# Performance work log

Measured on AMD Instinct MI355X. Metric: run time of the kernel, lower is better.

## Reference

```python
import jax, jax.numpy as jnp
import numpy as np

WH, WW = 7, 7
N = WH * WW
NH = 6
HEAD_DIM = 192 // NH
W_RES = 56
R_MAX = 4 * 56  # patch_size[0] * H
PI = 3.141592653589793


def _rel_coords():
    ch, cw = np.arange(WH), np.arange(WW)
    coords = np.stack(np.meshgrid(ch, cw, indexing='ij'))  # (2, WH, WW)
    flat = coords.reshape(2, -1)
    rel = flat[:, :, None] - flat[:, None, :]  # (2, N, N)
    radius = rel[0]   # in [-(WH-1), WH-1]
    azimuth = rel[1]  # in [-(WW-1), WW-1]
    return radius, azimuth


def setup_inputs() -> dict:
    key = jax.random.key(0)
    ks = jax.random.split(key, 10)
    B_ = 2048
    dim = 192
    return {
        'x': jax.random.normal(ks[0], (B_, N, dim), jnp.float32),
        'D': jax.random.uniform(ks[1], (B_, 1), jnp.float32),
        'qkv_w': jax.random.normal(ks[2], (3 * dim, dim), jnp.float32) * 0.02,
        'qkv_b': jax.random.normal(ks[3], (3 * dim,), jnp.float32) * 0.02,
        'proj_w': jax.random.normal(ks[4], (dim, dim), jnp.float32) * 0.02,
        'proj_b': jax.random.normal(ks[5], (dim,), jnp.float32) * 0.02,
        'a_p': jax.random.normal(ks[6], (2 * WW - 1, NH), jnp.float32) * 0.02,
        'b_p': jax.random.normal(ks[7], (2 * WW - 1, NH), jnp.float32) * 0.02,
        'a_r': jax.random.normal(ks[8], (2 * WH - 1, NH), jnp.float32) * 0.02,
        'b_r': jax.random.normal(ks[9], (2 * WH - 1, NH), jnp.float32) * 0.02,
    }


def reference(x, D, qkv_w, qkv_b, proj_w, proj_b, a_p, b_p, a_r, b_r):
    B_, n, C = x.shape
    radius_np, azimuth_np = _rel_coords()
    # torch a_r[radius] with negative ints wraps like python indexing; emulate via modulo
    rad_idx = jnp.asarray(radius_np % (2 * WH - 1))
    az_idx = jnp.asarray(azimuth_np % (2 * WW - 1))
    radius = jnp.asarray(radius_np, jnp.float32)   # (N, N)
    azimuth = jnp.asarray(azimuth_np, jnp.float32)  # (N, N)

    scale = HEAD_DIM ** -0.5
    qkv = (x @ qkv_w.T + qkv_b).reshape(B_, n, 3, NH, HEAD_DIM)
    qkv = jnp.transpose(qkv, (2, 0, 3, 1, 4))  # (3, B_, NH, N, hd)
    q, k, v = qkv[0] * scale, qkv[1], qkv[2]

    attn = jnp.einsum('bhnd,bhmd->bhnm', q, k)  # (B_, NH, N, N)

    # azimuthal bias: (N, N, NH) -> (NH, N, N)
    az = azimuth * (2.0 * PI / W_RES)
    A_phi = a_p[az_idx] * jnp.cos(az)[..., None] + b_p[az_idx] * jnp.sin(az)[..., None]
    A_phi = jnp.transpose(A_phi, (2, 0, 1))  # (NH, N, N)

    # radial bias: D (B_,1) scales radius -> (B_, N, N); combine -> (B_, NH, N, N)
    rad = D[:, 0][:, None, None] * radius[None]  # (B_, N, N)
    ang = rad * (2.0 * PI / R_MAX)
    A_r = (a_r[rad_idx][None] * jnp.cos(ang)[..., None]
           + b_r[rad_idx][None] * jnp.sin(ang)[..., None])  # (B_, N, N, NH)
    A_r = jnp.transpose(A_r, (0, 3, 1, 2))  # (B_, NH, N, N)

    attn = jax.nn.softmax(attn + A_phi[None] + A_r, axis=-1)
    out = jnp.einsum('bhnm,bhmd->bhnd', attn, v)
    out = jnp.transpose(out, (0, 2, 1, 3)).reshape(B_, n, C)
    return out @ proj_w.T + proj_b
```

## Files before the change

### kernel.cpp

```cpp
#include <hip/hip_runtime.h>

#define NTOK 49
#define NH 6
#define HD 32
#define DIM 192
#define QKV_DIM 576
#define PI_F 3.14159265358979323846f

typedef __bf16 bf16_t;
typedef __bf16 bf16x4 __attribute__((ext_vector_type(4)));
typedef __bf16 bf16x8 __attribute__((ext_vector_type(8)));
typedef float f32x4 __attribute__((ext_vector_type(4)));

__global__ __launch_bounds__(256) void cvt_weights(const float* __restrict__ qkv_w,
                                                   const float* __restrict__ proj_w,
                                                   bf16_t* __restrict__ wq,
                                                   bf16_t* __restrict__ wp) {
    int idx = blockIdx.x * 256 + threadIdx.x;
    if (idx < QKV_DIM * DIM) {
        wq[idx] = (bf16_t)qkv_w[idx];
    } else {
        int j = idx - QKV_DIM * DIM;
        if (j < DIM * DIM) wp[j] = (bf16_t)proj_w[j];
    }
}

__device__ __forceinline__ int2 pack4(float a, float b, float c, float d) {
    bf16x4 t = { (bf16_t)a, (bf16_t)b, (bf16_t)c, (bf16_t)d };
    union { bf16x4 v; int2 i; } u;
    u.v = t;
    return u.i;
}

__device__ __forceinline__ bf16x8 asm_frag(int2 p0, int2 p1, int src_lo, bool sel_hi) {
    int a0x = __shfl(p0.x, src_lo),      a0y = __shfl(p0.y, src_lo);
    int a1x = __shfl(p0.x, src_lo + 16), a1y = __shfl(p0.y, src_lo + 16);
    int b0x = __shfl(p1.x, src_lo),      b0y = __shfl(p1.y, src_lo);
    int b1x = __shfl(p1.x, src_lo + 16), b1y = __shfl(p1.y, src_lo + 16);
    union { int x[4]; bf16x8 v; } u;
    u.x[0] = sel_hi ? b0x : a0x;
    u.x[1] = sel_hi ? b0y : a0y;
    u.x[2] = sel_hi ? b1x : a1x;
    u.x[3] = sel_hi ? b1y : a1y;
    return u.v;
}

__global__ __launch_bounds__(384, 3) void fused_win_attn(
        const float* __restrict__ x,
        const float* __restrict__ Dp,
        const bf16_t* __restrict__ wq,
        const float* __restrict__ qkv_b,
        const bf16_t* __restrict__ wp,
        const float* __restrict__ proj_b,
        const float* __restrict__ a_p,
        const float* __restrict__ b_p,
        const float* __restrict__ a_r,
        const float* __restrict__ b_r,
        float* __restrict__ out) {
    __shared__ __align__(16) bf16_t sh_xo[49 * 200];
    __shared__ __align__(16) bf16_t vt_sh[NH][32 * 72];
    __shared__ float bias_sh[NH][169];

    const int tid  = threadIdx.x;
    const int w    = tid >> 6;
    const int lane = tid & 63;
    const int l16  = lane & 15;
    const int quad = lane >> 4;
    const int win  = blockIdx.x;

    bf16_t* vt     = vt_sh[w];
    float*  bias13 = bias_sh[w];

    const float* xg = x + (size_t)win * (NTOK * DIM);
    for (int u = tid; u < 2352; u += 384) {
        int e = u * 4;
        int r = e / 192, c = e % 192;
        float4 xv = *(const float4*)(xg + e);
        bf16x4 pk = { (bf16_t)xv.x, (bf16_t)xv.y, (bf16_t)xv.z, (bf16_t)xv.w };
        *(bf16x4*)(&sh_xo[r * 200 + c]) = pk;
    }

    const float Dv = Dp[win];
    for (int u = lane; u < 169; u += 64) {
        int dr = u / 13 - 6, da = u % 13 - 6;
        int ri = (dr < 0) ? dr + 13 : dr;
        int ai = (da < 0) ? da + 13 : da;
        float ang_a = (float)da * (2.0f * PI_F / 56.0f);
        float ang_r = Dv * (float)dr * (2.0f * PI_F / 448.0f);
        bias13[u] = a_p[ai * NH + w] * __cosf(ang_a) + b_p[ai * NH + w] * __sinf(ang_a)
                  + a_r[ri * NH + w] * __cosf(ang_r) + b_r[ri * NH + w] * __sinf(ang_r);
    }
    __syncthreads();

    int xoff[4];
#pragma unroll
    for (int mt = 0; mt < 4; ++mt) {
        int row = mt * 16 + l16;
        xoff[mt] = min(row, 48) * 200 + quad * 8;
    }

    const float scale = 0.17677669529663687f;
    int2 qp[4][2], kp[4][2];
    {
        const bf16_t* wgq = wq + (size_t)(w * 32) * DIM;
        const bf16_t* wgk = wq + (size_t)(DIM + w * 32) * DIM;
        f32x4 qa[4][2] = {}, ka[4][2] = {};
#pragma unroll
        for (int ks = 0; ks < 6; ++ks) {
            bf16x8 wq0 = *(const bf16x8*)(wgq + (size_t)l16 * DIM + ks * 32 + quad * 8);
            bf16x8 wq1 = *(const bf16x8*)(wgq + (size_t)(16 + l16) * DIM + ks * 32 + quad * 8);
            bf16x8 wk0 = *(const bf16x8*)(wgk + (size_t)l16 * DIM + ks * 32 + quad * 8);
            bf16x8 wk1 = *(const bf16x8*)(wgk + (size_t)(16 + l16) * DIM + ks * 32 + quad * 8);
#pragma unroll
            for (int mt = 0; mt < 4; ++mt) {
                bf16x8 xf = *(const bf16x8*)(&sh_xo[xoff[mt] + ks * 32]);
                qa[mt][0] = __builtin_amdgcn_mfma_f32_16x16x32_bf16(wq0, xf, qa[mt][0], 0, 0, 0);
                qa[mt][1] = __builtin_amdgcn_mfma_f32_16x16x32_bf16(wq1, xf, qa[mt][1], 0, 0, 0);
                ka[mt][0] = __builtin_amdgcn_mfma_f32_16x16x32_bf16(wk0, xf, ka[mt][0], 0, 0, 0);
                ka[mt][1] = __builtin_amdgcn_mfma_f32_16x16x32_bf16(wk1, xf, ka[mt][1], 0, 0, 0);
            }
        }
        float4 bq0 = *(const float4*)(qkv_b + w * 32 + quad * 4);
        float4 bq1 = *(const float4*)(qkv_b + w * 32 + 16 + quad * 4);
        float4 bk0 = *(const float4*)(qkv_b + DIM + w * 32 + quad * 4);
        float4 bk1 = *(const float4*)(qkv_b + DIM + w * 32 + 16 + quad * 4);
#pragma unroll
        for (int mt = 0; mt < 4; ++mt) {
            qp[mt][0] = pack4((qa[mt][0][0] + bq0.x) * scale, (qa[mt][0][1] + bq0.y) * scale,
                              (qa[mt][0][2] + bq0.z) * scale, (qa[mt][0][3] + bq0.w) * scale);
            qp[mt][1] = pack4((qa[mt][1][0] + bq1.x) * scale, (qa[mt][1][1] + bq1.y) * scale,
                              (qa[mt][1][2] + bq1.z) * scale, (qa[mt][1][3] + bq1.w) * scale);
            kp[mt][0] = pack4(ka[mt][0][0] + bk0.x, ka[mt][0][1] + bk0.y,
                              ka[mt][0][2] + bk0.z, ka[mt][0][3] + bk0.w);
            kp[mt][1] = pack4(ka[mt][1][0] + bk1.x, ka[mt][1][1] + bk1.y,
                              ka[mt][1][2] + bk1.z, ka[mt][1][3] + bk1.w);
        }
    }
    {
        const bf16_t* wgv = wq + (size_t)(2 * DIM + w * 32) * DIM;
        f32x4 va[4][2] = {};
#pragma unroll
        for (int ks = 0; ks < 6; ++ks) {
            bf16x8 wv0 = *(const bf16x8*)(wgv + (size_t)l16 * DIM + ks * 32 + quad * 8);
            bf16x8 wv1 = *(const bf16x8*)(wgv + (size_t)(16 + l16) * DIM + ks * 32 + quad * 8);
#pragma unroll
            for (int mt = 0; mt < 4; ++mt) {
                bf16x8 xf = *(const bf16x8*)(&sh_xo[xoff[mt] + ks * 32]);
                va[mt][0] = __builtin_amdgcn_mfma_f32_16x16x32_bf16(xf, wv0, va[mt][0], 0, 0, 0);
                va[mt][1] = __builtin_amdgcn_mfma_f32_16x16x32_bf16(xf, wv1, va[mt][1], 0, 0, 0);
            }
        }
        float bv0 = qkv_b[2 * DIM + w * 32 + l16];
        float bv1 = qkv_b[2 * DIM + w * 32 + 16 + l16];
#pragma unroll
        for (int mt = 0; mt < 4; ++mt) {
            *(int2*)(&vt[l16 * 72 + mt * 16 + quad * 4]) =
                pack4(va[mt][0][0] + bv0, va[mt][0][1] + bv0, va[mt][0][2] + bv0, va[mt][0][3] + bv0);
            *(int2*)(&vt[(16 + l16) * 72 + mt * 16 + quad * 4]) =
                pack4(va[mt][1][0] + bv1, va[mt][1][1] + bv1, va[mt][1][2] + bv1, va[mt][1][3] + bv1);
        }
    }

    const int src_lo  = ((lane >> 4) & 1) * 32 + l16;
    const bool sel_hi = (lane & 32) != 0;
    bf16x8 qf[4], kf[4];
#pragma unroll
    for (int t = 0; t < 4; ++t) {
        qf[t] = asm_frag(qp[t][0], qp[t][1], src_lo, sel_hi);
        kf[t] = asm_frag(kp[t][0], kp[t][1], src_lo, sel_hi);
    }
    bf16x8 vf[2][2];
#pragma unroll
    for (int ntd = 0; ntd < 2; ++ntd)
#pragma unroll
        for (int kt = 0; kt < 2; ++kt)
            vf[ntd][kt] = *(const bf16x8*)(&vt[(ntd * 16 + l16) * 72 + kt * 32 + quad * 8]);

    int jcp[4];
#pragma unroll
    for (int nt = 0; nt < 4; ++nt) {
        int p = 0;
#pragma unroll
        for (int r = 0; r < 4; ++r) {
            int j = nt * 16 + quad * 4 + r;
            p |= ((j / 7) * 13 + (j % 7)) << (8 * r);
        }
        jcp[nt] = p;
    }

    __syncthreads();

    for (int mt = 0; mt < 4; ++mt) {
        f32x4 s[4] = {};
#pragma unroll
        for (int nt = 0; nt < 4; ++nt)
            s[nt] = __builtin_amdgcn_mfma_f32_16x16x32_bf16(kf[nt], qf[mt], s[nt], 0, 0, 0);

        int i = mt * 16 + l16;
        int icl = min(i, 48);
        int icode = (icl / 7) * 13 + (icl % 7) + 84;

        float val[4][4];
        float mx = -1e30f;
#pragma unroll
        for (int nt = 0; nt < 4; ++nt)
#pragma unroll
            for (int r = 0; r < 4; ++r) {
                int j = nt * 16 + quad * 4 + r;
                int idx = icode - ((jcp[nt] >> (8 * r)) & 255);
                idx = max(idx, 0);
                float vv = s[nt][r] + bias13[idx];
                vv = (j < 49) ? vv : -1e30f;
                val[nt][r] = vv;
                mx = fmaxf(mx, vv);
            }
        mx = fmaxf(mx, __shfl_xor(mx, 16));
        mx = fmaxf(mx, __shfl_xor(mx, 32));
        float sum = 0.f;
#pragma unroll
        for (int nt = 0; nt < 4; ++nt)
#pragma unroll
            for (int r = 0; r < 4; ++r) {
                float e = __expf(val[nt][r] - mx);
                val[nt][r] = e;
                sum += e;
            }
        sum += __shfl_xor(sum, 16);
        sum += __shfl_xor(sum, 32);
        float rs = 1.0f / sum;

        int2 pv0 = pack4(val[0][0], val[0][1], val[0][2], val[0][3]);
        int2 pv1 = pack4(val[1][0], val[1][1], val[1][2], val[1][3]);
        int2 pv2 = pack4(val[2][0], val[2][1], val[2][2], val[2][3]);
        int2 pv3 = pack4(val[3][0], val[3][1], val[3][2], val[3][3]);
        bf16x8 pT0 = asm_frag(pv0, pv1, src_lo, sel_hi);
        bf16x8 pT1 = asm_frag(pv2, pv3, src_lo, sel_hi);

        f32x4 o0 = {}, o1 = {};
        o0 = __builtin_amdgcn_mfma_f32_16x16x32_bf16(vf[0][0], pT0, o0, 0, 0, 0);
        o0 = __builtin_amdgcn_mfma_f32_16x16x32_bf16(vf[0][1], pT1, o0, 0, 0, 0);
        o1 = __builtin_amdgcn_mfma_f32_16x16x32_bf16(vf[1][0], pT0, o1, 0, 0, 0);
        o1 = __builtin_amdgcn_mfma_f32_16x16x32_bf16(vf[1][1], pT1, o1, 0, 0, 0);

        if (i < 49) {
            *(int2*)(&sh_xo[i * 200 + w * 32 + quad * 4]) =
                pack4(o0[0] * rs, o0[1] * rs, o0[2] * rs, o0[3] * rs);
            *(int2*)(&sh_xo[i * 200 + w * 32 + 16 + quad * 4]) =
                pack4(o1[0] * rs, o1[1] * rs, o1[2] * rs, o1[3] * rs);
        }
    }

    __syncthreads();

    bf16x8 wf[2][6];
#pragma unroll
    for (int nt = 0; nt < 2; ++nt)
#pragma unroll
        for (int ks = 0; ks < 6; ++ks)
            wf[nt][ks] = *(const bf16x8*)(wp + (size_t)(w * 32 + nt * 16 + l16) * DIM + ks * 32 + quad * 8);

    f32x4 pacc[4][2] = {};
#pragma unroll
    for (int mt = 0; mt < 4; ++mt)
#pragma unroll
        for (int ks = 0; ks < 6; ++ks) {
            bf16x8 oa = *(const bf16x8*)(&sh_xo[xoff[mt] + ks * 32]);
            pacc[mt][0] = __builtin_amdgcn_mfma_f32_16x16x32_bf16(oa, wf[0][ks], pacc[mt][0], 0, 0, 0);
            pacc[mt][1] = __builtin_amdgcn_mfma_f32_16x16x32_bf16(oa, wf[1][ks], pacc[mt][1], 0, 0, 0);
        }

    float pb0 = proj_b[w * 32 + l16];
    float pb1 = proj_b[w * 32 + 16 + l16];
#pragma unroll
    for (int mt = 0; mt < 4; ++mt)
#pragma unroll
        for (int r = 0; r < 4; ++r) {
            int i = mt * 16 + quad * 4 + r;
            if (i < 49) {
                float* op = out + ((size_t)win * NTOK + i) * DIM + w * 32;
                op[l16]      = pacc[mt][0][r] + pb0;
                op[16 + l16] = pacc[mt][1][r] + pb1;
            }
        }
}

extern "C" void kernel_launch(void* const* d_in, const int* in_sizes, int n_in,
                              void* d_out, int out_size, void* d_ws, size_t ws_size,
                              hipStream_t stream) {
    const float* x      = (const float*)d_in[0];
    const float* D      = (const float*)d_in[1];
    const float* qkv_w  = (const float*)d_in[2];
    const float* qkv_b  = (const float*)d_in[3];
    const float* proj_w = (const float*)d_in[4];
    const float* proj_b = (const float*)d_in[5];
    const float* a_p    = (const float*)d_in[6];
    const float* b_p    = (const float*)d_in[7];
    const float* a_r    = (const float*)d_in[8];
    const float* b_r    = (const float*)d_in[9];
    float* out = (float*)d_out;

    const int B_ = in_sizes[0] / (NTOK * DIM);

    char* wsp = (char*)d_ws;
    bf16_t* wq = (bf16_t*)wsp; wsp += (size_t)QKV_DIM * DIM * 2;
    bf16_t* wp = (bf16_t*)wsp;

    cvt_weights<<<dim3((QKV_DIM * DIM + DIM * DIM + 255) / 256), dim3(256), 0, stream>>>(
        qkv_w, proj_w, wq, wp);

    fused_win_attn<<<dim3(B_), dim3(384), 0, stream>>>(
        x, D, wq, qkv_b, wp, proj_b, a_p, b_p, a_r, b_r, out);
}
```

Before: 302.6 us.

## Process two windows per 768-thread block and keep V fragments in registers

```diff
diff --git a/kernel.cpp b/kernel.cpp
--- a/kernel.cpp
+++ b/kernel.cpp
@@ -6,6 +6,7 @@
 #define DIM 192
 #define QKV_DIM 576
 #define PI_F 3.14159265358979323846f
+#define XSTR 204
 
 typedef __bf16 bf16_t;
 typedef __bf16 bf16x4 __attribute__((ext_vector_type(4)));
@@ -45,7 +46,7 @@
     return u.v;
 }
 
-__global__ __launch_bounds__(384, 3) void fused_win_attn(
+__global__ __launch_bounds__(768, 3) void fused_win_attn(
         const float* __restrict__ x,
         const float* __restrict__ Dp,
         const bf16_t* __restrict__ wq,
@@ -56,39 +57,44 @@
         const float* __restrict__ b_p,
         const float* __restrict__ a_r,
         const float* __restrict__ b_r,
-        float* __restrict__ out) {
-    __shared__ __align__(16) bf16_t sh_xo[49 * 200];
-    __shared__ __align__(16) bf16_t vt_sh[NH][32 * 72];
-    __shared__ float bias_sh[NH][169];
+        float* __restrict__ out,
+        int nwin) {
+    __shared__ __align__(16) bf16_t sh_xo[2][49 * XSTR];
+    __shared__ float bias_sh[12][169];
 
     const int tid  = threadIdx.x;
     const int w    = tid >> 6;
     const int lane = tid & 63;
     const int l16  = lane & 15;
     const int quad = lane >> 4;
-    const int win  = blockIdx.x;
-
-    bf16_t* vt     = vt_sh[w];
+    const int wb   = w / 6;
+    const int h    = w % 6;
+    const int win  = blockIdx.x * 2 + wb;
+    const int winc = min(win, nwin - 1);
+    const bool alive = (win < nwin);
+
+    bf16_t* xl     = sh_xo[wb];
     float*  bias13 = bias_sh[w];
 
-    const float* xg = x + (size_t)win * (NTOK * DIM);
-    for (int u = tid; u < 2352; u += 384) {
-        int e = u * 4;
+    for (int u = tid; u < 4704; u += 768) {
+        int wbs = (u >= 2352) ? 1 : 0;
+        int e = (u - wbs * 2352) * 4;
         int r = e / 192, c = e % 192;
-        float4 xv = *(const float4*)(xg + e);
+        int wsrc = min(blockIdx.x * 2 + wbs, nwin - 1);
+        float4 xv = *(const float4*)(x + (size_t)wsrc * (NTOK * DIM) + e);
         bf16x4 pk = { (bf16_t)xv.x, (bf16_t)xv.y, (bf16_t)xv.z, (bf16_t)xv.w };
-        *(bf16x4*)(&sh_xo[r * 200 + c]) = pk;
-    }
-
-    const float Dv = Dp[win];
+        *(bf16x4*)(&sh_xo[wbs][r * XSTR + c]) = pk;
+    }
+
+    const float Dv = Dp[winc];
     for (int u = lane; u < 169; u += 64) {
         int dr = u / 13 - 6, da = u % 13 - 6;
         int ri = (dr < 0) ? dr + 13 : dr;
         int ai = (da < 0) ? da + 13 : da;
         float ang_a = (float)da * (2.0f * PI_F / 56.0f);
         float ang_r = Dv * (float)dr * (2.0f * PI_F / 448.0f);
-        bias13[u] = a_p[ai * NH + w] * __cosf(ang_a) + b_p[ai * NH + w] * __sinf(ang_a)
-                  + a_r[ri * NH + w] * __cosf(ang_r) + b_r[ri * NH + w] * __sinf(ang_r);
+        bias13[u] = a_p[ai * NH + h] * __cosf(ang_a) + b_p[ai * NH + h] * __sinf(ang_a)
+                  + a_r[ri * NH + h] * __cosf(ang_r) + b_r[ri * NH + h] * __sinf(ang_r);
     }
     __syncthreads();
 
@@ -96,14 +102,17 @@
 #pragma unroll
     for (int mt = 0; mt < 4; ++mt) {
         int row = mt * 16 + l16;
-        xoff[mt] = min(row, 48) * 200 + quad * 8;
-    }
+        xoff[mt] = min(row, 48) * XSTR + quad * 8;
+    }
+
+    const int src_lo  = ((lane >> 4) & 1) * 32 + l16;
+    const bool sel_hi = (lane & 32) != 0;
 
     const float scale = 0.17677669529663687f;
     int2 qp[4][2], kp[4][2];
     {
-        const bf16_t* wgq = wq + (size_t)(w * 32) * DIM;
-        const bf16_t* wgk = wq + (size_t)(DIM + w * 32) * DIM;
+        const bf16_t* wgq = wq + (size_t)(h * 32) * DIM;
+        const bf16_t* wgk = wq + (size_t)(DIM + h * 32) * DIM;
         f32x4 qa[4][2] = {}, ka[4][2] = {};
 #pragma unroll
         for (int ks = 0; ks < 6; ++ks) {
@@ -113,17 +122,17 @@
             bf16x8 wk1 = *(const bf16x8*)(wgk + (size_t)(16 + l16) * DIM + ks * 32 + quad * 8);
 #pragma unroll
             for (int mt = 0; mt < 4; ++mt) {
-                bf16x8 xf = *(const bf16x8*)(&sh_xo[xoff[mt] + ks * 32]);
+                bf16x8 xf = *(const bf16x8*)(&xl[xoff[mt] + ks * 32]);
                 qa[mt][0] = __builtin_amdgcn_mfma_f32_16x16x32_bf16(wq0, xf, qa[mt][0], 0, 0, 0);
                 qa[mt][1] = __builtin_amdgcn_mfma_f32_16x16x32_bf16(wq1, xf, qa[mt][1], 0, 0, 0);
                 ka[mt][0] = __builtin_amdgcn_mfma_f32_16x16x32_bf16(wk0, xf, ka[mt][0], 0, 0, 0);
                 ka[mt][1] = __builtin_amdgcn_mfma_f32_16x16x32_bf16(wk1, xf, ka[mt][1], 0, 0, 0);
             }
         }
-        float4 bq0 = *(const float4*)(qkv_b + w * 32 + quad * 4);
-        float4 bq1 = *(const float4*)(qkv_b + w * 32 + 16 + quad * 4);
-        float4 bk0 = *(const float4*)(qkv_b + DIM + w * 32 + quad * 4);
-        float4 bk1 = *(const float4*)(qkv_b + DIM + w * 32 + 16 + quad * 4);
+        float4 bq0 = *(const float4*)(qkv_b + h * 32 + quad * 4);
+        float4 bq1 = *(const float4*)(qkv_b + h * 32 + 16 + quad * 4);
+        float4 bk0 = *(const float4*)(qkv_b + DIM + h * 32 + quad * 4);
+        float4 bk1 = *(const float4*)(qkv_b + DIM + h * 32 + 16 + quad * 4);
 #pragma unroll
         for (int mt = 0; mt < 4; ++mt) {
             qp[mt][0] = pack4((qa[mt][0][0] + bq0.x) * scale, (qa[mt][0][1] + bq0.y) * scale,
@@ -136,8 +145,10 @@
                               ka[mt][1][2] + bk1.z, ka[mt][1][3] + bk1.w);
         }
     }
+
+    int2 vp[4][2];
     {
-        const bf16_t* wgv = wq + (size_t)(2 * DIM + w * 32) * DIM;
+        const bf16_t* wgv = wq + (size_t)(2 * DIM + h * 32) * DIM;
         f32x4 va[4][2] = {};
 #pragma unroll
         for (int ks = 0; ks < 6; ++ks) {
@@ -145,24 +156,22 @@
             bf16x8 wv1 = *(const bf16x8*)(wgv + (size_t)(16 + l16) * DIM + ks * 32 + quad * 8);
 #pragma unroll
             for (int mt = 0; mt < 4; ++mt) {
-                bf16x8 xf = *(const bf16x8*)(&sh_xo[xoff[mt] + ks * 32]);
+                bf16x8 xf = *(const bf16x8*)(&xl[xoff[mt] + ks * 32]);
                 va[mt][0] = __builtin_amdgcn_mfma_f32_16x16x32_bf16(xf, wv0, va[mt][0], 0, 0, 0);
                 va[mt][1] = __builtin_amdgcn_mfma_f32_16x16x32_bf16(xf, wv1, va[mt][1], 0, 0, 0);
             }
         }
-        float bv0 = qkv_b[2 * DIM + w * 32 + l16];
-        float bv1 = qkv_b[2 * DIM + w * 32 + 16 + l16];
+        float bv0 = qkv_b[2 * DIM + h * 32 + l16];
+        float bv1 = qkv_b[2 * DIM + h * 32 + 16 + l16];
 #pragma unroll
         for (int mt = 0; mt < 4; ++mt) {
-            *(int2*)(&vt[l16 * 72 + mt * 16 + quad * 4]) =
-                pack4(va[mt][0][0] + bv0, va[mt][0][1] + bv0, va[mt][0][2] + bv0, va[mt][0][3] + bv0);
-            *(int2*)(&vt[(16 + l16) * 72 + mt * 16 + quad * 4]) =
-                pack4(va[mt][1][0] + bv1, va[mt][1][1] + bv1, va[mt][1][2] + bv1, va[mt][1][3] + bv1);
-        }
-    }
-
-    const int src_lo  = ((lane >> 4) & 1) * 32 + l16;
-    const bool sel_hi = (lane & 32) != 0;
+            vp[mt][0] = pack4(va[mt][0][0] + bv0, va[mt][0][1] + bv0,
+                              va[mt][0][2] + bv0, va[mt][0][3] + bv0);
+            vp[mt][1] = pack4(va[mt][1][0] + bv1, va[mt][1][1] + bv1,
+                              va[mt][1][2] + bv1, va[mt][1][3] + bv1);
+        }
+    }
+
     bf16x8 qf[4], kf[4];
 #pragma unroll
     for (int t = 0; t < 4; ++t) {
@@ -171,10 +180,10 @@
     }
     bf16x8 vf[2][2];
 #pragma unroll
-    for (int ntd = 0; ntd < 2; ++ntd)
-#pragma unroll
-        for (int kt = 0; kt < 2; ++kt)
-            vf[ntd][kt] = *(const bf16x8*)(&vt[(ntd * 16 + l16) * 72 + kt * 32 + quad * 8]);
+    for (int kt = 0; kt < 2; ++kt)
+#pragma unroll
+        for (int ntd = 0; ntd < 2; ++ntd)
+            vf[ntd][kt] = asm_frag(vp[2 * kt][ntd], vp[2 * kt + 1][ntd], src_lo, sel_hi);
 
     int jcp[4];
 #pragma unroll
@@ -243,9 +252,9 @@
         o1 = __builtin_amdgcn_mfma_f32_16x16x32_bf16(vf[1][1], pT1, o1, 0, 0, 0);
 
         if (i < 49) {
-            *(int2*)(&sh_xo[i * 200 + w * 32 + quad * 4]) =
+            *(int2*)(&xl[i * XSTR + h * 32 + quad * 4]) =
                 pack4(o0[0] * rs, o0[1] * rs, o0[2] * rs, o0[3] * rs);
-            *(int2*)(&sh_xo[i * 200 + w * 32 + 16 + quad * 4]) =
+            *(int2*)(&xl[i * XSTR + h * 32 + 16 + quad * 4]) =
                 pack4(o1[0] * rs, o1[1] * rs, o1[2] * rs, o1[3] * rs);
         }
     }
@@ -257,27 +266,27 @@
     for (int nt = 0; nt < 2; ++nt)
 #pragma unroll
         for (int ks = 0; ks < 6; ++ks)
-            wf[nt][ks] = *(const bf16x8*)(wp + (size_t)(w * 32 + nt * 16 + l16) * DIM + ks * 32 + quad * 8);
+            wf[nt][ks] = *(const bf16x8*)(wp + (size_t)(h * 32 + nt * 16 + l16) * DIM + ks * 32 + quad * 8);
 
     f32x4 pacc[4][2] = {};
 #pragma unroll
     for (int mt = 0; mt < 4; ++mt)
 #pragma unroll
         for (int ks = 0; ks < 6; ++ks) {
-            bf16x8 oa = *(const bf16x8*)(&sh_xo[xoff[mt] + ks * 32]);
+            bf16x8 oa = *(const bf16x8*)(&xl[xoff[mt] + ks * 32]);
             pacc[mt][0] = __builtin_amdgcn_mfma_f32_16x16x32_bf16(oa, wf[0][ks], pacc[mt][0], 0, 0, 0);
             pacc[mt][1] = __builtin_amdgcn_mfma_f32_16x16x32_bf16(oa, wf[1][ks], pacc[mt][1], 0, 0, 0);
         }
 
-    float pb0 = proj_b[w * 32 + l16];
-    float pb1 = proj_b[w * 32 + 16 + l16];
+    float pb0 = proj_b[h * 32 + l16];
+    float pb1 = proj_b[h * 32 + 16 + l16];
 #pragma unroll
     for (int mt = 0; mt < 4; ++mt)
 #pragma unroll
         for (int r = 0; r < 4; ++r) {
             int i = mt * 16 + quad * 4 + r;
-            if (i < 49) {
-                float* op = out + ((size_t)win * NTOK + i) * DIM + w * 32;
+            if (alive && i < 49) {
+                float* op = out + ((size_t)win * NTOK + i) * DIM + h * 32;
                 op[l16]      = pacc[mt][0][r] + pb0;
                 op[16 + l16] = pacc[mt][1][r] + pb1;
             }
@@ -308,6 +317,6 @@
     cvt_weights<<<dim3((QKV_DIM * DIM + DIM * DIM + 255) / 256), dim3(256), 0, stream>>>(
         qkv_w, proj_w, wq, wp);
 
-    fused_win_attn<<<dim3(B_), dim3(384), 0, stream>>>(
-        x, D, wq, qkv_b, wp, proj_b, a_p, b_p, a_r, b_r, out);
-}
+    fused_win_attn<<<dim3((B_ + 1) / 2), dim3(768), 0, stream>>>(
+        x, D, wq, qkv_b, wp, proj_b, a_p, b_p, a_r, b_r, out, B_);
+}
```

Measured after the change: 295.6 us. -2.3%, faster.
